# Performance work log

Measured on AMD Instinct MI355X. Metric: run time of the kernel, lower is better.

Reference implementation:

```python
import jax, jax.numpy as jnp
import numpy as np

N, E, H, C = 50000, 1_600_000, 4, 32
DIN, DE = 128, 32
NEG_SLOPE = 0.2  # PyG GATConv leaky_relu negative_slope default


def setup_inputs() -> dict:
    key = jax.random.key(0)
    ks = jax.random.split(key, 12)
    s = 0.1  # weight scale
    return {
        "x": jax.random.normal(ks[0], (N, DIN), jnp.float32),
        "edge_index": jax.random.randint(ks[1], (2, E), 0, N, jnp.int32),
        "edge_attr": jax.random.normal(ks[2], (E, DE), jnp.float32),
        "W": jax.random.normal(ks[3], (DIN, H * C), jnp.float32) * s,
        "att_src": jax.random.normal(ks[4], (H, C), jnp.float32) * s,
        "att_dst": jax.random.normal(ks[5], (H, C), jnp.float32) * s,
        "lin_edge_W": jax.random.normal(ks[6], (DE, H * C), jnp.float32) * s,
        "att_edge": jax.random.normal(ks[7], (H, C), jnp.float32) * s,
        "bias": jax.random.normal(ks[8], (H * C,), jnp.float32) * s,
        "proj_W": jax.random.normal(ks[9], (H * C, C), jnp.float32) * s,
        "proj_b": jax.random.normal(ks[10], (C,), jnp.float32) * s,
    }


def reference(x, edge_index, edge_attr, W, att_src, att_dst, lin_edge_W,
              att_edge, bias, proj_W, proj_b):
    n = x.shape[0]
    h, c = att_src.shape
    src, dst = edge_index[0], edge_index[1]

    # add self loops; loop edge_attr = mean of incoming edge_attr (PyG fill_value='mean')
    deg = jax.ops.segment_sum(jnp.ones(src.shape, x.dtype), dst, num_segments=n)
    ea_mean = jax.ops.segment_sum(edge_attr, dst, num_segments=n) / jnp.maximum(deg, 1.0)[:, None]
    loop = jnp.arange(n, dtype=src.dtype)
    src = jnp.concatenate([src, loop])
    dst = jnp.concatenate([dst, loop])
    ea = jnp.concatenate([edge_attr, ea_mean], axis=0)

    xl = (x @ W).reshape(n, h, c)                       # [N,H,C]
    a_src = jnp.einsum('nhc,hc->nh', xl, att_src)       # [N,H]
    a_dst = jnp.einsum('nhc,hc->nh', xl, att_dst)
    e = (ea @ lin_edge_W).reshape(-1, h, c)             # [E',H,C]
    a_e = jnp.einsum('ehc,hc->eh', e, att_edge)

    alpha = jax.nn.leaky_relu(a_src[src] + a_dst[dst] + a_e, NEG_SLOPE)  # [E',H]
    amax = jax.lax.stop_gradient(jax.ops.segment_max(alpha, dst, num_segments=n))
    alpha = jnp.exp(alpha - amax[dst])
    denom = jax.ops.segment_sum(alpha, dst, num_segments=n)
    alpha = alpha / (denom[dst] + 1e-16)                # segment softmax over incoming edges

    out = jax.ops.segment_sum(xl[src] * alpha[..., None], dst, num_segments=n)  # [N,H,C]
    out = out.reshape(n, h * c) + bias                  # concat heads + bias
    return out @ proj_W + proj_b                        # concat projection
```

## Files before the change

kernel.cpp:

```cpp
#include <hip/hip_runtime.h>

#define NEG_SLOPE 0.2f

__device__ __forceinline__ float lrelu(float x) { return x > 0.0f ? x : NEG_SLOPE * x; }

__device__ __forceinline__ float bcast(float v, int srcLane) {
  return __int_as_float(__builtin_amdgcn_readlane(__float_as_int(v), srcLane));
}

__device__ __forceinline__ unsigned pack_bf16(float a, float b) {
  unsigned ua = __float_as_uint(a), ub = __float_as_uint(b);
  ua += 0x7fffu + ((ua >> 16) & 1u);
  ub += 0x7fffu + ((ub >> 16) & 1u);
  return (ua >> 16) | (ub & 0xffff0000u);
}
__device__ __forceinline__ float bf16lo(unsigned z) { return __uint_as_float(z << 16); }
__device__ __forceinline__ float bf16hi(unsigned z) { return __uint_as_float(z & 0xffff0000u); }

__global__ void k0_setup(const float* __restrict__ W, const float* __restrict__ proj_W,
                         const float* __restrict__ att_src, const float* __restrict__ att_dst,
                         const float* __restrict__ lin_edge_W, const float* __restrict__ att_edge,
                         const float* __restrict__ bias, const float* __restrict__ proj_b,
                         float* __restrict__ Wz, float* __restrict__ Ws, float* __restrict__ Wd,
                         float* __restrict__ M, float* __restrict__ cproj) {
  int t = blockIdx.x * blockDim.x + threadIdx.x;
  if (t < 16384) {
    int d = t >> 7, o = t & 127;
    int h = o >> 5, jj = o & 31;
    float s = 0.f;
    #pragma unroll
    for (int c = 0; c < 32; ++c)
      s += W[d * 128 + h * 32 + c] * proj_W[(h * 32 + c) * 32 + jj];
    Wz[d * 128 + o] = s;
  } else if (t < 16384 + 512) {
    int idx = t - 16384; int d = idx >> 2, h = idx & 3;
    float s = 0.f;
    #pragma unroll
    for (int c = 0; c < 32; ++c) s += W[d * 128 + h * 32 + c] * att_src[h * 32 + c];
    Ws[d * 4 + h] = s;
  } else if (t < 16384 + 1024) {
    int idx = t - 16384 - 512; int d = idx >> 2, h = idx & 3;
    float s = 0.f;
    #pragma unroll
    for (int c = 0; c < 32; ++c) s += W[d * 128 + h * 32 + c] * att_dst[h * 32 + c];
    Wd[d * 4 + h] = s;
  } else if (t < 16384 + 1024 + 128) {
    int idx = t - 16384 - 1024; int d = idx >> 2, h = idx & 3;
    float s = 0.f;
    #pragma unroll
    for (int c = 0; c < 32; ++c) s += lin_edge_W[d * 128 + h * 32 + c] * att_edge[h * 32 + c];
    M[d * 4 + h] = s;
  } else if (t < 16384 + 1024 + 128 + 32) {
    int jj = t - 16384 - 1024 - 128;
    float s = proj_b[jj];
    #pragma unroll
    for (int k = 0; k < 128; ++k) s += bias[k] * proj_W[k * 32 + jj];
    cproj[jj] = s;
  }
}

__global__ __launch_bounds__(256) void k3_gemm(
    const float* __restrict__ x, const float* __restrict__ Wz,
    const float* __restrict__ Ws, const float* __restrict__ Wd,
    int n, unsigned* __restrict__ Zp, float* __restrict__ a_src, float* __restrict__ a_dst) {
  __shared__ float2 Wl[128 * 64];
  int tid = threadIdx.x;
  for (int idx = tid; idx < 128 * 64; idx += 256) {
    int k = idx >> 6, l = idx & 63;
    Wl[idx] = make_float2(Wz[k * 128 + l], Wz[k * 128 + 64 + l]);
  }
  __syncthreads();
  int lane = tid & 63, wid = tid >> 6;
  float ws0[4], ws1[4], wd0[4], wd1[4];
  #pragma unroll
  for (int h = 0; h < 4; ++h) {
    ws0[h] = Ws[lane * 4 + h];  ws1[h] = Ws[(64 + lane) * 4 + h];
    wd0[h] = Wd[lane * 4 + h];  wd1[h] = Wd[(64 + lane) * 4 + h];
  }
  int gw = blockIdx.x * 4 + wid;
  int nw = gridDim.x * 4;
  for (int base = gw * 4; base < n; base += nw * 4) {
    float xa[4], xb[4];
    #pragma unroll
    for (int u = 0; u < 4; ++u) {
      int node = base + u;
      xa[u] = (node < n) ? x[node * 128 + lane] : 0.0f;
      xb[u] = (node < n) ? x[node * 128 + 64 + lane] : 0.0f;
    }
    float acc0[4] = {0.f, 0.f, 0.f, 0.f}, acc1[4] = {0.f, 0.f, 0.f, 0.f};
    #pragma unroll 16
    for (int k = 0; k < 64; ++k) {
      float2 w = Wl[k * 64 + lane];
      #pragma unroll
      for (int u = 0; u < 4; ++u) {
        float xv = bcast(xa[u], k);
        acc0[u] += xv * w.x; acc1[u] += xv * w.y;
      }
    }
    #pragma unroll 16
    for (int k = 0; k < 64; ++k) {
      float2 w = Wl[(64 + k) * 64 + lane];
      #pragma unroll
      for (int u = 0; u < 4; ++u) {
        float xv = bcast(xb[u], k);
        acc0[u] += xv * w.x; acc1[u] += xv * w.y;
      }
    }
    #pragma unroll
    for (int u = 0; u < 4; ++u) {
      int node = base + u;
      if (node >= n) break;
      Zp[(size_t)node * 64 + lane] = pack_bf16(acc0[u], acc1[u]);
      float ps[4], pd[4];
      #pragma unroll
      for (int h = 0; h < 4; ++h) {
        ps[h] = xa[u] * ws0[h] + xb[u] * ws1[h];
        pd[h] = xa[u] * wd0[h] + xb[u] * wd1[h];
      }
      #pragma unroll
      for (int m = 1; m < 64; m <<= 1) {
        #pragma unroll
        for (int h = 0; h < 4; ++h) {
          ps[h] += __shfl_xor(ps[h], m);
          pd[h] += __shfl_xor(pd[h], m);
        }
      }
      if (lane == 0) {
        *(float4*)&a_src[node * 4] = make_float4(ps[0], ps[1], ps[2], ps[3]);
        *(float4*)&a_dst[node * 4] = make_float4(pd[0], pd[1], pd[2], pd[3]);
      }
    }
  }
}

__global__ __launch_bounds__(256) void k1_edge(
    const int* __restrict__ ei, int E, const float4* __restrict__ ea4,
    const float* __restrict__ Mg,
    const float* __restrict__ a_src, const float* __restrict__ a_dst,
    uint4* __restrict__ we, int* __restrict__ deg, int* __restrict__ rank) {
  __shared__ float4 s_ea[256 * 9];
  __shared__ float4 Msh[32];
  int t = threadIdx.x;
  if (t < 32) Msh[t] = ((const float4*)Mg)[t];
  int B0 = blockIdx.x * 256;
  #pragma unroll
  for (int k = 0; k < 8; ++k) {
    int f = k * 256 + t;
    int e = B0 + (f >> 3);
    float4 v = (e < E) ? ea4[(size_t)B0 * 8 + f] : make_float4(0.f, 0.f, 0.f, 0.f);
    s_ea[(f >> 3) * 9 + (f & 7)] = v;
  }
  __syncthreads();
  int e = B0 + t;
  if (e >= E) return;
  int s = ei[e], d = ei[E + e];
  float4 as = *(const float4*)&a_src[(size_t)s * 4];
  float4 ad = *(const float4*)&a_dst[(size_t)d * 4];
  float ae0 = 0.f, ae1 = 0.f, ae2 = 0.f, ae3 = 0.f;
  #pragma unroll
  for (int j = 0; j < 8; ++j) {
    float4 v = s_ea[t * 9 + j];
    float4 m0 = Msh[j * 4 + 0], m1 = Msh[j * 4 + 1], m2 = Msh[j * 4 + 2], m3 = Msh[j * 4 + 3];
    ae0 += v.x * m0.x + v.y * m1.x + v.z * m2.x + v.w * m3.x;
    ae1 += v.x * m0.y + v.y * m1.y + v.z * m2.y + v.w * m3.y;
    ae2 += v.x * m0.z + v.y * m1.z + v.z * m2.z + v.w * m3.z;
    ae3 += v.x * m0.w + v.y * m1.w + v.z * m2.w + v.w * m3.w;
  }
  float w0 = __expf(lrelu(ae0 + as.x + ad.x));
  float w1 = __expf(lrelu(ae1 + as.y + ad.y));
  float w2 = __expf(lrelu(ae2 + as.z + ad.z));
  float w3 = __expf(lrelu(ae3 + as.w + ad.w));
  we[e] = make_uint4(pack_bf16(w0, w1), pack_bf16(w2, w3),
                     pack_bf16(ae0, ae1), pack_bf16(ae2, ae3));
  rank[e] = atomicAdd(&deg[d], 1);
}

__global__ void k2_scan(const int* __restrict__ deg, int n, int* __restrict__ offsets) {
  __shared__ int shw[16];
  __shared__ int shtot;
  int tid = threadIdx.x;
  int lane = tid & 63, wid = tid >> 6;
  int running = 0;
  for (int base = 0; base < n; base += 4096) {
    int i = base + tid * 4;
    int4 v = make_int4(0, 0, 0, 0);
    if (i + 3 < n) v = *(const int4*)&deg[i];
    else {
      if (i < n) v.x = deg[i];
      if (i + 1 < n) v.y = deg[i + 1];
      if (i + 2 < n) v.z = deg[i + 2];
      if (i + 3 < n) v.w = deg[i + 3];
    }
    int tsum = v.x + v.y + v.z + v.w;
    int inc = tsum;
    #pragma unroll
    for (int s = 1; s < 64; s <<= 1) {
      int t = __shfl_up(inc, s);
      if (lane >= s) inc += t;
    }
    if (lane == 63) shw[wid] = inc;
    __syncthreads();
    if (wid == 0) {
      int w = (lane < 16) ? shw[lane] : 0;
      int winc = w;
      #pragma unroll
      for (int s = 1; s < 16; s <<= 1) {
        int t = __shfl_up(winc, s);
        if (lane >= s) winc += t;
      }
      if (lane < 16) shw[lane] = winc - w;
      if (lane == 15) shtot = winc;
    }
    __syncthreads();
    int excl = running + shw[wid] + inc - tsum;
    if (i < n)     offsets[i + 1] = excl + v.x;
    if (i + 1 < n) offsets[i + 2] = excl + v.x + v.y;
    if (i + 2 < n) offsets[i + 3] = excl + v.x + v.y + v.z;
    if (i + 3 < n) offsets[i + 4] = excl + tsum;
    running += shtot;
    __syncthreads();
  }
  if (tid == 0) offsets[0] = 0;
}

__global__ void k4_scatter(const int* __restrict__ ei, int E,
                           const int* __restrict__ rank, const int* __restrict__ offsets,
                           const uint4* __restrict__ we, uint4* __restrict__ csr) {
  int e = blockIdx.x * blockDim.x + threadIdx.x;
  if (e >= E) return;
  int s = ei[e], d = ei[E + e];
  int slot = offsets[d] + rank[e];
  uint4 w = we[e];
  uint4* ent = &csr[(size_t)slot * 2];
  *(int*)ent = s;
  ent[1] = w;
}

__global__ __launch_bounds__(256) void k5_agg(
    const int* __restrict__ offsets, const uint4* __restrict__ csr,
    const unsigned* __restrict__ Zp,
    const float* __restrict__ a_src, const float* __restrict__ a_dst,
    const float* __restrict__ cproj, int n, float* __restrict__ out) {
  __shared__ float4 s_w[4][64];
  __shared__ int    s_s[4][64];
  int tid = threadIdx.x;
  int lane = tid & 63, wid = tid >> 6;
  int gw = blockIdx.x * 4 + wid, nw = gridDim.x * 4;
  int h0 = lane >> 5, j = lane & 31;
  float cp = cproj[j];
  const float* wbase = (const float*)&s_w[wid][0];
  for (int node = gw; node < n; node += nw) {
    int off0 = offsets[node], off1 = offsets[node + 1];
    int dg = off1 - off0;
    float dsx = 0.f, dsy = 0.f, dsz = 0.f, dsw = 0.f;
    float aex = 0.f, aey = 0.f, aez = 0.f, aew = 0.f;
    float agg0 = 0.f, agg1 = 0.f;
    for (int base = off0; base < off1; base += 64) {
      int rem = off1 - base; if (rem > 64) rem = 64;
      if (lane < rem) {
        const uint4* ent = &csr[(size_t)(base + lane) * 2];
        int s = *(const int*)ent;
        uint4 w = ent[1];
        float w0 = bf16lo(w.x), w1 = bf16hi(w.x);
        float w2 = bf16lo(w.y), w3 = bf16hi(w.y);
        dsx += w0; dsy += w1; dsz += w2; dsw += w3;
        aex += bf16lo(w.z); aey += bf16hi(w.z);
        aez += bf16lo(w.w); aew += bf16hi(w.w);
        s_w[wid][lane] = make_float4(w0, w2, w1, w3);
        s_s[wid][lane] = s;
      }
      int jj = 0;
      for (; jj + 4 <= rem; jj += 4) {
        int s0 = s_s[wid][jj], s1 = s_s[wid][jj + 1];
        int s2 = s_s[wid][jj + 2], s3 = s_s[wid][jj + 3];
        unsigned z0 = Zp[(size_t)s0 * 64 + lane];
        unsigned z1 = Zp[(size_t)s1 * 64 + lane];
        unsigned z2 = Zp[(size_t)s2 * 64 + lane];
        unsigned z3 = Zp[(size_t)s3 * 64 + lane];
        float2 w0 = *(const float2*)(wbase + (jj    ) * 4 + 2 * h0);
        float2 w1 = *(const float2*)(wbase + (jj + 1) * 4 + 2 * h0);
        float2 w2 = *(const float2*)(wbase + (jj + 2) * 4 + 2 * h0);
        float2 w3 = *(const float2*)(wbase + (jj + 3) * 4 + 2 * h0);
        agg0 += w0.x * bf16lo(z0) + w1.x * bf16lo(z1) + w2.x * bf16lo(z2) + w3.x * bf16lo(z3);
        agg1 += w0.y * bf16hi(z0) + w1.y * bf16hi(z1) + w2.y * bf16hi(z2) + w3.y * bf16hi(z3);
      }
      for (; jj < rem; ++jj) {
        int s0 = s_s[wid][jj];
        unsigned z0 = Zp[(size_t)s0 * 64 + lane];
        float2 w0 = *(const float2*)(wbase + jj * 4 + 2 * h0);
        agg0 += w0.x * bf16lo(z0);
        agg1 += w0.y * bf16hi(z0);
      }
    }
    #pragma unroll
    for (int m = 1; m < 64; m <<= 1) {
      dsx += __shfl_xor(dsx, m); dsy += __shfl_xor(dsy, m);
      dsz += __shfl_xor(dsz, m); dsw += __shfl_xor(dsw, m);
      aex += __shfl_xor(aex, m); aey += __shfl_xor(aey, m);
      aez += __shfl_xor(aez, m); aew += __shfl_xor(aew, m);
    }
    float invd = 1.0f / (float)(dg > 0 ? dg : 1);
    float4 asn = *(const float4*)&a_src[node * 4];
    float4 ad  = *(const float4*)&a_dst[node * 4];
    float w0 = __expf(lrelu(asn.x + ad.x + aex * invd));
    float w1 = __expf(lrelu(asn.y + ad.y + aey * invd));
    float w2 = __expf(lrelu(asn.z + ad.z + aez * invd));
    float w3 = __expf(lrelu(asn.w + ad.w + aew * invd));
    dsx += w0; dsy += w1; dsz += w2; dsw += w3;
    unsigned zpn = Zp[(size_t)node * 64 + lane];
    float sw0 = h0 ? w1 : w0, sw1 = h0 ? w3 : w2;
    agg0 += sw0 * bf16lo(zpn);
    agg1 += sw1 * bf16hi(zpn);
    float d0 = h0 ? dsy : dsx, d1 = h0 ? dsw : dsz;
    float tt = agg0 / (d0 + 1e-16f) + agg1 / (d1 + 1e-16f);
    tt += __shfl_xor(tt, 32);
    if (lane < 32) out[node * 32 + j] = tt + cp;
  }
}

extern "C" void kernel_launch(void* const* d_in, const int* in_sizes, int n_in,
                              void* d_out, int out_size, void* d_ws, size_t ws_size,
                              hipStream_t stream) {
  const float* x          = (const float*)d_in[0];
  const int*   ei         = (const int*)  d_in[1];
  const float* ea         = (const float*)d_in[2];
  const float* W          = (const float*)d_in[3];
  const float* att_src    = (const float*)d_in[4];
  const float* att_dst    = (const float*)d_in[5];
  const float* lin_edge_W = (const float*)d_in[6];
  const float* att_edge   = (const float*)d_in[7];
  const float* bias       = (const float*)d_in[8];
  const float* proj_W     = (const float*)d_in[9];
  const float* proj_b     = (const float*)d_in[10];
  float* out = (float*)d_out;
  int N = in_sizes[0] / 128;
  int E = in_sizes[1] / 2;

  char* p = (char*)d_ws;
  auto alloc = [&](size_t bytes) {
    char* r = p;
    p += (bytes + 255) & ~(size_t)255;
    return r;
  };
  unsigned* Zp     = (unsigned*)alloc((size_t)N * 64 * 4);
  float* a_src     = (float*)alloc((size_t)N * 4 * 4);
  float* a_dst     = (float*)alloc((size_t)N * 4 * 4);
  int*   deg       = (int*)  alloc((size_t)N * 4);
  int*   offsets   = (int*)  alloc((size_t)(N + 1) * 4);
  int*   rank      = (int*)  alloc((size_t)E * 4);
  uint4* we        = (uint4*)alloc((size_t)E * 16);
  uint4* csr       = (uint4*)alloc((size_t)E * 32);
  float* Wz        = (float*)alloc(128 * 128 * 4);
  float* Ws        = (float*)alloc(128 * 4 * 4);
  float* Wd        = (float*)alloc(128 * 4 * 4);
  float* M         = (float*)alloc(32 * 4 * 4);
  float* cproj     = (float*)alloc(32 * 4);

  hipMemsetAsync(deg, 0, (size_t)N * 4, stream);

  k0_setup<<<69, 256, 0, stream>>>(W, proj_W, att_src, att_dst, lin_edge_W, att_edge,
                                   bias, proj_b, Wz, Ws, Wd, M, cproj);
  k3_gemm<<<512, 256, 0, stream>>>(x, Wz, Ws, Wd, N, Zp, a_src, a_dst);
  k1_edge<<<(E + 255) / 256, 256, 0, stream>>>(ei, E, (const float4*)ea, M,
                                               a_src, a_dst, we, deg, rank);
  k2_scan<<<1, 1024, 0, stream>>>(deg, N, offsets);
  k4_scatter<<<(E + 255) / 256, 256, 0, stream>>>(ei, E, rank, offsets, we, csr);
  k5_agg<<<2048, 256, 0, stream>>>(offsets, csr, Zp, a_src, a_dst, cproj, N, out);
}
```

Measured before the change: 558.2 us.

## Build CSR before edge pass and write compact 16-byte entries directly

Degree counting and the prefix scan now run first in a small atomic-only kernel. The edge-attention kernel can then write each edge's result straight into its final CSR slot, so the intermediate per-edge buffer and the separate scatter kernel are gone. The CSR entry shrinks from 32 to 16 bytes by packing the source index, the bf16 attention weights and 8-bit fixed-point edge logits into one uint4. This cuts global traffic in the edge, scatter and aggregation phases. The trade-off is the 8-bit quantization of the edge logits used for the self-loop mean, which adds error and clips values outside about ±4.

```diff
diff --git a/kernel.cpp b/kernel.cpp
--- a/kernel.cpp
+++ b/kernel.cpp
@@ -16,6 +16,15 @@
 }
 __device__ __forceinline__ float bf16lo(unsigned z) { return __uint_as_float(z << 16); }
 __device__ __forceinline__ float bf16hi(unsigned z) { return __uint_as_float(z & 0xffff0000u); }
+
+__device__ __forceinline__ unsigned quant8(float a) {
+  int q = (int)rintf(a * 32.0f) + 128;
+  q = q < 0 ? 0 : (q > 255 ? 255 : q);
+  return (unsigned)q;
+}
+__device__ __forceinline__ float dequant8(unsigned q) {
+  return ((int)q - 128) * (1.0f / 32.0f);
+}
 
 __global__ void k0_setup(const float* __restrict__ W, const float* __restrict__ proj_W,
                          const float* __restrict__ att_src, const float* __restrict__ att_dst,
@@ -59,120 +68,10 @@
   }
 }
 
-__global__ __launch_bounds__(256) void k3_gemm(
-    const float* __restrict__ x, const float* __restrict__ Wz,
-    const float* __restrict__ Ws, const float* __restrict__ Wd,
-    int n, unsigned* __restrict__ Zp, float* __restrict__ a_src, float* __restrict__ a_dst) {
-  __shared__ float2 Wl[128 * 64];
-  int tid = threadIdx.x;
-  for (int idx = tid; idx < 128 * 64; idx += 256) {
-    int k = idx >> 6, l = idx & 63;
-    Wl[idx] = make_float2(Wz[k * 128 + l], Wz[k * 128 + 64 + l]);
-  }
-  __syncthreads();
-  int lane = tid & 63, wid = tid >> 6;
-  float ws0[4], ws1[4], wd0[4], wd1[4];
-  #pragma unroll
-  for (int h = 0; h < 4; ++h) {
-    ws0[h] = Ws[lane * 4 + h];  ws1[h] = Ws[(64 + lane) * 4 + h];
-    wd0[h] = Wd[lane * 4 + h];  wd1[h] = Wd[(64 + lane) * 4 + h];
-  }
-  int gw = blockIdx.x * 4 + wid;
-  int nw = gridDim.x * 4;
-  for (int base = gw * 4; base < n; base += nw * 4) {
-    float xa[4], xb[4];
-    #pragma unroll
-    for (int u = 0; u < 4; ++u) {
-      int node = base + u;
-      xa[u] = (node < n) ? x[node * 128 + lane] : 0.0f;
-      xb[u] = (node < n) ? x[node * 128 + 64 + lane] : 0.0f;
-    }
-    float acc0[4] = {0.f, 0.f, 0.f, 0.f}, acc1[4] = {0.f, 0.f, 0.f, 0.f};
-    #pragma unroll 16
-    for (int k = 0; k < 64; ++k) {
-      float2 w = Wl[k * 64 + lane];
-      #pragma unroll
-      for (int u = 0; u < 4; ++u) {
-        float xv = bcast(xa[u], k);
-        acc0[u] += xv * w.x; acc1[u] += xv * w.y;
-      }
-    }
-    #pragma unroll 16
-    for (int k = 0; k < 64; ++k) {
-      float2 w = Wl[(64 + k) * 64 + lane];
-      #pragma unroll
-      for (int u = 0; u < 4; ++u) {
-        float xv = bcast(xb[u], k);
-        acc0[u] += xv * w.x; acc1[u] += xv * w.y;
-      }
-    }
-    #pragma unroll
-    for (int u = 0; u < 4; ++u) {
-      int node = base + u;
-      if (node >= n) break;
-      Zp[(size_t)node * 64 + lane] = pack_bf16(acc0[u], acc1[u]);
-      float ps[4], pd[4];
-      #pragma unroll
-      for (int h = 0; h < 4; ++h) {
-        ps[h] = xa[u] * ws0[h] + xb[u] * ws1[h];
-        pd[h] = xa[u] * wd0[h] + xb[u] * wd1[h];
-      }
-      #pragma unroll
-      for (int m = 1; m < 64; m <<= 1) {
-        #pragma unroll
-        for (int h = 0; h < 4; ++h) {
-          ps[h] += __shfl_xor(ps[h], m);
-          pd[h] += __shfl_xor(pd[h], m);
-        }
-      }
-      if (lane == 0) {
-        *(float4*)&a_src[node * 4] = make_float4(ps[0], ps[1], ps[2], ps[3]);
-        *(float4*)&a_dst[node * 4] = make_float4(pd[0], pd[1], pd[2], pd[3]);
-      }
-    }
-  }
-}
-
-__global__ __launch_bounds__(256) void k1_edge(
-    const int* __restrict__ ei, int E, const float4* __restrict__ ea4,
-    const float* __restrict__ Mg,
-    const float* __restrict__ a_src, const float* __restrict__ a_dst,
-    uint4* __restrict__ we, int* __restrict__ deg, int* __restrict__ rank) {
-  __shared__ float4 s_ea[256 * 9];
-  __shared__ float4 Msh[32];
-  int t = threadIdx.x;
-  if (t < 32) Msh[t] = ((const float4*)Mg)[t];
-  int B0 = blockIdx.x * 256;
-  #pragma unroll
-  for (int k = 0; k < 8; ++k) {
-    int f = k * 256 + t;
-    int e = B0 + (f >> 3);
-    float4 v = (e < E) ? ea4[(size_t)B0 * 8 + f] : make_float4(0.f, 0.f, 0.f, 0.f);
-    s_ea[(f >> 3) * 9 + (f & 7)] = v;
-  }
-  __syncthreads();
-  int e = B0 + t;
-  if (e >= E) return;
-  int s = ei[e], d = ei[E + e];
-  float4 as = *(const float4*)&a_src[(size_t)s * 4];
-  float4 ad = *(const float4*)&a_dst[(size_t)d * 4];
-  float ae0 = 0.f, ae1 = 0.f, ae2 = 0.f, ae3 = 0.f;
-  #pragma unroll
-  for (int j = 0; j < 8; ++j) {
-    float4 v = s_ea[t * 9 + j];
-    float4 m0 = Msh[j * 4 + 0], m1 = Msh[j * 4 + 1], m2 = Msh[j * 4 + 2], m3 = Msh[j * 4 + 3];
-    ae0 += v.x * m0.x + v.y * m1.x + v.z * m2.x + v.w * m3.x;
-    ae1 += v.x * m0.y + v.y * m1.y + v.z * m2.y + v.w * m3.y;
-    ae2 += v.x * m0.z + v.y * m1.z + v.z * m2.z + v.w * m3.z;
-    ae3 += v.x * m0.w + v.y * m1.w + v.z * m2.w + v.w * m3.w;
-  }
-  float w0 = __expf(lrelu(ae0 + as.x + ad.x));
-  float w1 = __expf(lrelu(ae1 + as.y + ad.y));
-  float w2 = __expf(lrelu(ae2 + as.z + ad.z));
-  float w3 = __expf(lrelu(ae3 + as.w + ad.w));
-  we[e] = make_uint4(pack_bf16(w0, w1), pack_bf16(w2, w3),
-                     pack_bf16(ae0, ae1), pack_bf16(ae2, ae3));
-  rank[e] = atomicAdd(&deg[d], 1);
+__global__ void k1_count(const int* __restrict__ dst, int E, int* __restrict__ deg,
+                         int* __restrict__ rank) {
+  int i = blockIdx.x * blockDim.x + threadIdx.x;
+  if (i < E) rank[i] = atomicAdd(&deg[dst[i]], 1);
 }
 
 __global__ void k2_scan(const int* __restrict__ deg, int n, int* __restrict__ offsets) {
@@ -223,17 +122,121 @@
   if (tid == 0) offsets[0] = 0;
 }
 
-__global__ void k4_scatter(const int* __restrict__ ei, int E,
-                           const int* __restrict__ rank, const int* __restrict__ offsets,
-                           const uint4* __restrict__ we, uint4* __restrict__ csr) {
-  int e = blockIdx.x * blockDim.x + threadIdx.x;
+__global__ __launch_bounds__(256) void k3_gemm(
+    const float* __restrict__ x, const float* __restrict__ Wz,
+    const float* __restrict__ Ws, const float* __restrict__ Wd,
+    int n, unsigned* __restrict__ Zp, float* __restrict__ a_src, float* __restrict__ a_dst) {
+  __shared__ float2 Wl[128 * 64];
+  int tid = threadIdx.x;
+  for (int idx = tid; idx < 128 * 64; idx += 256) {
+    int k = idx >> 6, l = idx & 63;
+    Wl[idx] = make_float2(Wz[k * 128 + l], Wz[k * 128 + 64 + l]);
+  }
+  __syncthreads();
+  int lane = tid & 63, wid = tid >> 6;
+  float ws0[4], ws1[4], wd0[4], wd1[4];
+  #pragma unroll
+  for (int h = 0; h < 4; ++h) {
+    ws0[h] = Ws[lane * 4 + h];  ws1[h] = Ws[(64 + lane) * 4 + h];
+    wd0[h] = Wd[lane * 4 + h];  wd1[h] = Wd[(64 + lane) * 4 + h];
+  }
+  int gw = blockIdx.x * 4 + wid;
+  int nw = gridDim.x * 4;
+  for (int base = gw * 4; base < n; base += nw * 4) {
+    float xa[4], xb[4];
+    #pragma unroll
+    for (int u = 0; u < 4; ++u) {
+      int node = base + u;
+      xa[u] = (node < n) ? x[node * 128 + lane] : 0.0f;
+      xb[u] = (node < n) ? x[node * 128 + 64 + lane] : 0.0f;
+    }
+    float acc0[4] = {0.f, 0.f, 0.f, 0.f}, acc1[4] = {0.f, 0.f, 0.f, 0.f};
+    #pragma unroll 16
+    for (int k = 0; k < 64; ++k) {
+      float2 w = Wl[k * 64 + lane];
+      #pragma unroll
+      for (int u = 0; u < 4; ++u) {
+        float xv = bcast(xa[u], k);
+        acc0[u] += xv * w.x; acc1[u] += xv * w.y;
+      }
+    }
+    #pragma unroll 16
+    for (int k = 0; k < 64; ++k) {
+      float2 w = Wl[(64 + k) * 64 + lane];
+      #pragma unroll
+      for (int u = 0; u < 4; ++u) {
+        float xv = bcast(xb[u], k);
+        acc0[u] += xv * w.x; acc1[u] += xv * w.y;
+      }
+    }
+    #pragma unroll
+    for (int u = 0; u < 4; ++u) {
+      int node = base + u;
+      if (node >= n) break;
+      Zp[(size_t)node * 64 + lane] = pack_bf16(acc0[u], acc1[u]);
+      float ps[4], pd[4];
+      #pragma unroll
+      for (int h = 0; h < 4; ++h) {
+        ps[h] = xa[u] * ws0[h] + xb[u] * ws1[h];
+        pd[h] = xa[u] * wd0[h] + xb[u] * wd1[h];
+      }
+      #pragma unroll
+      for (int m = 1; m < 64; m <<= 1) {
+        #pragma unroll
+        for (int h = 0; h < 4; ++h) {
+          ps[h] += __shfl_xor(ps[h], m);
+          pd[h] += __shfl_xor(pd[h], m);
+        }
+      }
+      if (lane == 0) {
+        *(float4*)&a_src[node * 4] = make_float4(ps[0], ps[1], ps[2], ps[3]);
+        *(float4*)&a_dst[node * 4] = make_float4(pd[0], pd[1], pd[2], pd[3]);
+      }
+    }
+  }
+}
+
+__global__ __launch_bounds__(256, 4) void k4_edge(
+    const int* __restrict__ ei, int E, const float4* __restrict__ ea4,
+    const float* __restrict__ Mg,
+    const float* __restrict__ a_src, const float* __restrict__ a_dst,
+    const int* __restrict__ rank, const int* __restrict__ offsets,
+    uint4* __restrict__ csr) {
+  __shared__ float4 s_ea[256 * 9];
+  __shared__ float4 Msh[32];
+  int t = threadIdx.x;
+  if (t < 32) Msh[t] = ((const float4*)Mg)[t];
+  int B0 = blockIdx.x * 256;
+  #pragma unroll
+  for (int k = 0; k < 8; ++k) {
+    int f = k * 256 + t;
+    int e = B0 + (f >> 3);
+    float4 v = (e < E) ? ea4[(size_t)B0 * 8 + f] : make_float4(0.f, 0.f, 0.f, 0.f);
+    s_ea[(f >> 3) * 9 + (f & 7)] = v;
+  }
+  __syncthreads();
+  int e = B0 + t;
   if (e >= E) return;
   int s = ei[e], d = ei[E + e];
+  float4 as = *(const float4*)&a_src[(size_t)s * 4];
+  float4 ad = *(const float4*)&a_dst[(size_t)d * 4];
   int slot = offsets[d] + rank[e];
-  uint4 w = we[e];
-  uint4* ent = &csr[(size_t)slot * 2];
-  *(int*)ent = s;
-  ent[1] = w;
+  float ae0 = 0.f, ae1 = 0.f, ae2 = 0.f, ae3 = 0.f;
+  #pragma unroll
+  for (int j = 0; j < 8; ++j) {
+    float4 v = s_ea[t * 9 + j];
+    float4 m0 = Msh[j * 4 + 0], m1 = Msh[j * 4 + 1], m2 = Msh[j * 4 + 2], m3 = Msh[j * 4 + 3];
+    ae0 += v.x * m0.x + v.y * m1.x + v.z * m2.x + v.w * m3.x;
+    ae1 += v.x * m0.y + v.y * m1.y + v.z * m2.y + v.w * m3.y;
+    ae2 += v.x * m0.z + v.y * m1.z + v.z * m2.z + v.w * m3.z;
+    ae3 += v.x * m0.w + v.y * m1.w + v.z * m2.w + v.w * m3.w;
+  }
+  float w0 = __expf(lrelu(ae0 + as.x + ad.x));
+  float w1 = __expf(lrelu(ae1 + as.y + ad.y));
+  float w2 = __expf(lrelu(ae2 + as.z + ad.z));
+  float w3 = __expf(lrelu(ae3 + as.w + ad.w));
+  unsigned aeq = quant8(ae0) | (quant8(ae1) << 8) | (quant8(ae2) << 16) | (quant8(ae3) << 24);
+  csr[slot] = make_uint4((unsigned)s, pack_bf16(w0, w1), pack_bf16(w2, w3), aeq);
 }
 
 __global__ __launch_bounds__(256) void k5_agg(
@@ -258,14 +261,15 @@
     for (int base = off0; base < off1; base += 64) {
       int rem = off1 - base; if (rem > 64) rem = 64;
       if (lane < rem) {
-        const uint4* ent = &csr[(size_t)(base + lane) * 2];
-        int s = *(const int*)ent;
-        uint4 w = ent[1];
-        float w0 = bf16lo(w.x), w1 = bf16hi(w.x);
-        float w2 = bf16lo(w.y), w3 = bf16hi(w.y);
+        uint4 ent = csr[(size_t)(base + lane)];
+        int s = (int)ent.x;
+        float w0 = bf16lo(ent.y), w1 = bf16hi(ent.y);
+        float w2 = bf16lo(ent.z), w3 = bf16hi(ent.z);
         dsx += w0; dsy += w1; dsz += w2; dsw += w3;
-        aex += bf16lo(w.z); aey += bf16hi(w.z);
-        aez += bf16lo(w.w); aew += bf16hi(w.w);
+        aex += dequant8(ent.w & 255u);
+        aey += dequant8((ent.w >> 8) & 255u);
+        aez += dequant8((ent.w >> 16) & 255u);
+        aew += dequant8(ent.w >> 24);
         s_w[wid][lane] = make_float4(w0, w2, w1, w3);
         s_s[wid][lane] = s;
       }
@@ -348,8 +352,7 @@
   int*   deg       = (int*)  alloc((size_t)N * 4);
   int*   offsets   = (int*)  alloc((size_t)(N + 1) * 4);
   int*   rank      = (int*)  alloc((size_t)E * 4);
-  uint4* we        = (uint4*)alloc((size_t)E * 16);
-  uint4* csr       = (uint4*)alloc((size_t)E * 32);
+  uint4* csr       = (uint4*)alloc((size_t)E * 16);
   float* Wz        = (float*)alloc(128 * 128 * 4);
   float* Ws        = (float*)alloc(128 * 4 * 4);
   float* Wd        = (float*)alloc(128 * 4 * 4);
@@ -360,10 +363,10 @@
 
   k0_setup<<<69, 256, 0, stream>>>(W, proj_W, att_src, att_dst, lin_edge_W, att_edge,
                                    bias, proj_b, Wz, Ws, Wd, M, cproj);
+  k1_count<<<(E + 255) / 256, 256, 0, stream>>>(ei + E, E, deg, rank);
+  k2_scan<<<1, 1024, 0, stream>>>(deg, N, offsets);
   k3_gemm<<<512, 256, 0, stream>>>(x, Wz, Ws, Wd, N, Zp, a_src, a_dst);
-  k1_edge<<<(E + 255) / 256, 256, 0, stream>>>(ei, E, (const float4*)ea, M,
-                                               a_src, a_dst, we, deg, rank);
-  k2_scan<<<1, 1024, 0, stream>>>(deg, N, offsets);
-  k4_scatter<<<(E + 255) / 256, 256, 0, stream>>>(ei, E, rank, offsets, we, csr);
+  k4_edge<<<(E + 255) / 256, 256, 0, stream>>>(ei, E, (const float4*)ea, M,
+                                               a_src, a_dst, rank, offsets, csr);
   k5_agg<<<2048, 256, 0, stream>>>(offsets, csr, Zp, a_src, a_dst, cproj, N, out);
 }
```

Measured after the change: 582.4 us. 1.04x slower.
